# Optimization experiments

Hardware: AMD Instinct MI355X
Metric: run time of the kernel (lower is better)

## Reference

```python
import jax, jax.numpy as jnp
import numpy as np

N = 768          # n_nuclei
EMB = 32         # embedding_dim
RBF = 32         # rbf_dim
CUTOFF = 10.0    # rbf_cutoff
MAXQ = 10        # max(charges)


def _edges(n):
    # fully-connected edge list exactly as in GNN.__call__
    senders = np.arange(n).repeat(n - 1)
    recv = np.arange(n)[None].repeat(n - 1, axis=0)
    recv = (recv + np.arange(n - 1)[:, None] + 1) % n
    return jnp.asarray(senders), jnp.asarray(recv.reshape(-1))


def _mlp2(x, w0, b0, w1, b1=None):
    # AutoMLP(out_dim, depth=2): Dense+silu, Dense (final_bias optional)
    h = jax.nn.silu(x @ w0 + b0)
    y = h @ w1
    return y if b1 is None else y + b1


def _seg_mean(vals, seg, n):
    s = jax.ops.segment_sum(vals, seg, num_segments=n, indices_are_sorted=True)
    c = jax.ops.segment_sum(jnp.ones((vals.shape[0], 1), vals.dtype), seg,
                            num_segments=n, indices_are_sorted=True)
    return s / jnp.maximum(c, 1.0)


def setup_inputs() -> dict:
    key = jax.random.key(0)
    ki = iter(jax.random.split(key, 48))

    def W(din, dout):
        return jax.random.normal(next(ki), (din, dout), jnp.float32) / np.sqrt(din).astype(np.float32)

    def b(d):
        return jax.random.normal(next(ki), (d,), jnp.float32) * 0.01

    return dict(
        nuclei=jax.random.normal(next(ki), (N, 3), jnp.float32) * 3.0,
        charges=jax.random.randint(next(ki), (N,), 0, MAXQ),
        f=(jnp.arange(RBF, dtype=jnp.float32) + 1.0) * jnp.pi,  # BesselRBF param init
        embed_table=jax.random.normal(next(ki), (MAXQ, EMB), jnp.float32),
        mp1_w0=W(96, 32), mp1_b0=b(32), mp1_w1=W(32, 32), mp1_b1=b(32),
        up1_w0=W(64, 64), up1_b0=b(64), up1_w1=W(64, 64), up1_b1=b(64),
        mp2_w0=W(160, 32), mp2_b0=b(32), mp2_w1=W(32, 32), mp2_b1=b(32),
        up2_w0=W(96, 64), up2_b0=b(64), up2_w1=W(64, 64), up2_b1=b(64),
        no_w0=W(160, 3), no_b0=b(3), no_w1=W(3, 3),
        no_embed=jax.random.normal(next(ki), (MAXQ, 3), jnp.float32) * 0.1,
        go_w0=W(160, 1), go_b0=b(1), go_w1=W(1, 1), go_b1=b(1),
    )


def reference(nuclei, charges, f, embed_table,
              mp1_w0, mp1_b0, mp1_w1, mp1_b1,
              up1_w0, up1_b0, up1_w1, up1_b1,
              mp2_w0, mp2_b0, mp2_w1, mp2_b1,
              up2_w0, up2_b0, up2_w1, up2_b1,
              no_w0, no_b0, no_w1, no_embed,
              go_w0, go_b0, go_w1, go_b1):
    nuclei = nuclei.reshape(-1, 3) @ jnp.eye(3, dtype=nuclei.dtype)  # constants 'axes'
    n = nuclei.shape[0]
    senders, receivers = _edges(n)

    # BesselRBF on pairwise distances
    d = jnp.linalg.norm(nuclei[senders] - nuclei[receivers], axis=-1)
    x_ext = d[:, None] + 1e-8
    e_embed = jnp.sqrt(2.0 / CUTOFF) * jnp.sin(f * x_ext / CUTOFF) / x_ext  # [E, RBF]

    n_embed = embed_table[charges]  # [N, EMB]
    embeddings = [n_embed]

    # layer 1: msg out 32, update out 64 (no residual: 32 != 64)
    edge_in = jnp.concatenate([n_embed[senders], n_embed[receivers], e_embed], axis=-1)
    msg = _seg_mean(_mlp2(edge_in, mp1_w0, mp1_b0, mp1_w1, mp1_b1), senders, n)
    upd = _mlp2(jnp.concatenate([n_embed, msg], axis=-1), up1_w0, up1_b0, up1_w1, up1_b1)
    n_embed = upd  # dims differ -> plain replacement
    embeddings.append(n_embed)

    # layer 2: msg out 32, update out 64 (residual: 64 == 64)
    edge_in = jnp.concatenate([n_embed[senders], n_embed[receivers], e_embed], axis=-1)
    msg = _seg_mean(_mlp2(edge_in, mp2_w0, mp2_b0, mp2_w1, mp2_b1), senders, n)
    upd = _mlp2(jnp.concatenate([n_embed, msg], axis=-1), up2_w0, up2_b0, up2_w1, up2_b1)
    n_embed = n_embed + upd
    embeddings.append(n_embed)

    agg = jnp.concatenate(embeddings, axis=-1)  # [N, 32+64+64=160]

    node_out = _mlp2(agg, no_w0, no_b0, no_w1) + no_embed[charges]  # [N, 3]
    global_out = _mlp2(jnp.mean(agg, axis=0), go_w0, go_b0, go_w1, go_b1)  # [1]
    return (node_out, global_out)
```

## Files before the change

kernel.cpp:

```cpp
#include <hip/hip_runtime.h>
#include <hip/hip_bf16.h>

typedef __hip_bfloat16 bf16;
typedef __attribute__((ext_vector_type(8))) short short8;
typedef __attribute__((ext_vector_type(4))) float float4v;

#define NN   768
#define NEPS 767

#define C_NUC   0
#define C_F     2304
#define C_ETAB  2336
#define C_MP1W0 2656
#define C_MP1B0 5728
#define C_MP1W1 5760
#define C_MP1B1 6784
#define C_UP1W0 6816
#define C_UP1B0 10912
#define C_UP1W1 10976
#define C_UP1B1 15072
#define C_MP2W0 15136
#define C_MP2B0 20256
#define C_MP2W1 20288
#define C_MP2B1 21312
#define C_UP2W0 21344
#define C_UP2B0 27488
#define C_UP2W1 27552
#define C_UP2B1 31648
#define C_NOW0  31712
#define C_NOB0  32192
#define C_NOW1  32195
#define C_NOEMB 32204
#define C_GOW0  32234
#define C_GOB0  32394
#define C_GOW1  32395
#define C_GOB1  32396
__device__ float g_c[32400];

#define OFF_EMB0 0
#define OFF_SA1  24576
#define OFF_SB1  49152
#define OFF_MSG1 73728
#define OFF_EMB1 98304
#define OFF_SA2  147456
#define OFF_SB2  172032
#define OFF_MSG2 196608
__device__ float g_ws[221184];
__device__ float g_agg[160];
__device__ int   g_cnt;
__device__ int   g_isf;

struct Ptrs { const void* p[28]; };

__device__ __forceinline__ float b2f(bf16 v){ return __bfloat162float(v); }
__device__ __forceinline__ float LD(const void* p, int i, int f32){
  return f32 ? ((const float*)p)[i] : b2f(((const bf16*)p)[i]);
}
__device__ __forceinline__ int detect_f32(const void* f){
  float v = ((const float*)f)[0];
  return (fabsf(v - 3.14159265f) < 0.01f) ? 1 : 0;
}
__device__ __forceinline__ float fast_rcp(float x){ return __builtin_amdgcn_rcpf(x); }
__device__ __forceinline__ float silu_f(float p){ return p * fast_rcp(1.f + __expf(-p)); }
__device__ __forceinline__ unsigned short rne_bf16(float x){
  unsigned int b = __float_as_uint(x);
  return (unsigned short)((b + 0x7fffu + ((b >> 16) & 1u)) >> 16);
}
__device__ __forceinline__ void cv(const void* p, int off, int sz, int gt, int isf){
  for (int i = gt; i < sz; i += 96*256) g_c[off + i] = LD(p, i, isf);
}

__launch_bounds__(256)
__global__ void k_conv_prep(Ptrs P, const int* __restrict__ charges){
  int t = threadIdx.x;
  int gt = blockIdx.x*256 + t;
  int isf = detect_f32(P.p[2]);
  if (gt == 0){ g_isf = isf; g_cnt = 0; }
  if (gt < 160) g_agg[gt] = 0.f;

  cv(P.p[0],  C_NUC,   2304, gt, isf);
  cv(P.p[2],  C_F,     32,   gt, isf);
  cv(P.p[3],  C_ETAB,  320,  gt, isf);
  cv(P.p[4],  C_MP1W0, 3072, gt, isf);
  cv(P.p[5],  C_MP1B0, 32,   gt, isf);
  cv(P.p[6],  C_MP1W1, 1024, gt, isf);
  cv(P.p[7],  C_MP1B1, 32,   gt, isf);
  cv(P.p[8],  C_UP1W0, 4096, gt, isf);
  cv(P.p[9],  C_UP1B0, 64,   gt, isf);
  cv(P.p[10], C_UP1W1, 4096, gt, isf);
  cv(P.p[11], C_UP1B1, 64,   gt, isf);
  cv(P.p[12], C_MP2W0, 5120, gt, isf);
  cv(P.p[13], C_MP2B0, 32,   gt, isf);
  cv(P.p[14], C_MP2W1, 1024, gt, isf);
  cv(P.p[15], C_MP2B1, 32,   gt, isf);
  cv(P.p[16], C_UP2W0, 6144, gt, isf);
  cv(P.p[17], C_UP2B0, 64,   gt, isf);
  cv(P.p[18], C_UP2W1, 4096, gt, isf);
  cv(P.p[19], C_UP2B1, 64,   gt, isf);
  cv(P.p[20], C_NOW0,  480,  gt, isf);
  cv(P.p[21], C_NOB0,  3,    gt, isf);
  cv(P.p[22], C_NOW1,  9,    gt, isf);
  cv(P.p[23], C_NOEMB, 30,   gt, isf);
  cv(P.p[24], C_GOW0,  160,  gt, isf);
  cv(P.p[25], C_GOB0,  1,    gt, isf);
  cv(P.p[26], C_GOW1,  1,    gt, isf);
  cv(P.p[27], C_GOB1,  1,    gt, isf);

  __shared__ float w0L[2048];
  __shared__ float rowL[8][32];
  for (int idx = t; idx < 2048; idx += 256) w0L[idx] = LD(P.p[4], idx, isf);
  int nd = t >> 5, col = t & 31;
  int node = blockIdx.x*8 + nd;
  int ch = charges[node];
  float v = LD(P.p[3], ch*32 + col, isf);
  g_ws[OFF_EMB0 + node*32 + col] = v;
  rowL[nd][col] = v;
  __syncthreads();
  float sa = 0.f, sb = 0.f;
  #pragma unroll
  for (int k = 0; k < 32; k++){
    float rv = rowL[nd][k];
    sa = fmaf(rv, w0L[k*32 + col],      sa);
    sb = fmaf(rv, w0L[(32+k)*32 + col], sb);
  }
  g_ws[OFF_SA1 + node*32 + col] = sa;
  g_ws[OFF_SB1 + node*32 + col] = sb;
}

__launch_bounds__(256)
__global__ void k_edge(int sa_off, int sb_off, int w0e_off, int b0_off,
                       int w1_off, int b1_off, int msg_off)
{
  __shared__ __align__(16) float pos[NN*3];
  __shared__ __align__(16) float w1L[1024];
  __shared__ float wsum[4][32];
  __shared__ float hsumL[32];

  int i = blockIdx.x, t = threadIdx.x;
  int w = t >> 6, lane = t & 63, q = lane >> 4, c = lane & 15;
  const float* SA = g_ws + sa_off;
  const float* SB = g_ws + sb_off;

  {
    const float4* src = (const float4*)(g_c + C_NUC);
    float4* dst = (float4*)pos;
    for (int idx = t; idx < 576; idx += 256) dst[idx] = src[idx];
    ((float4*)w1L)[t] = ((const float4*)(g_c + w1_off))[t];
  }
  short8 bf0, bf1;
  #pragma unroll
  for (int j = 0; j < 8; j++){
    int row = q*8 + j;
    bf0[j] = (short)rne_bf16(g_c[w0e_off + row*32 + c]);
    bf1[j] = (short)rne_bf16(g_c[w0e_off + row*32 + 16 + c]);
  }
  float preB0 = SA[i*32 + c]      + g_c[b0_off + c];
  float preB1 = SA[i*32 + 16 + c] + g_c[b0_off + 16 + c];
  float fj[8];
  #pragma unroll
  for (int j = 0; j < 8; j++) fj[j] = g_c[C_F + q*8 + j] * 0.1f;
  __syncthreads();

  float px = pos[i*3], py = pos[i*3+1], pz = pos[i*3+2];
  float sum0 = 0.f, sum1 = 0.f;

  for (int tl = w; tl < 48; tl += 4){
    int el = tl*16 + c;
    int ela = (el < NEPS) ? el : 0;
    int r = ela + (ela >= i);
    float dx = px - pos[r*3], dy = py - pos[r*3+1], dz = pz - pos[r*3+2];
    float d  = sqrtf(fmaf(dx, dx, fmaf(dy, dy, dz*dz)));
    float xs = d + 1e-8f;
    float sc = 0.44721359549995793f * fast_rcp(xs);
    short8 af;
    #pragma unroll
    for (int j = 0; j < 8; j++) af[j] = (short)rne_bf16(sc * __sinf(fj[j]*xs));

    float4v z = {0.f, 0.f, 0.f, 0.f};
    float4v a0 = __builtin_amdgcn_mfma_f32_16x16x32_bf16(af, bf0, z, 0, 0, 0);
    float4v a1 = __builtin_amdgcn_mfma_f32_16x16x32_bf16(af, bf1, z, 0, 0, 0);

    #pragma unroll
    for (int p = 0; p < 4; p++){
      int el2 = tl*16 + q*4 + p;
      if (el2 < NEPS){
        int r2 = el2 + (el2 >= i);
        float v0 = a0[p] + preB0 + SB[r2*32 + c];
        float v1 = a1[p] + preB1 + SB[r2*32 + 16 + c];
        sum0 += silu_f(v0);
        sum1 += silu_f(v1);
      }
    }
  }
  sum0 += __shfl_xor(sum0, 16); sum0 += __shfl_xor(sum0, 32);
  sum1 += __shfl_xor(sum1, 16); sum1 += __shfl_xor(sum1, 32);
  if (lane < 16){ wsum[w][lane] = sum0; wsum[w][16 + lane] = sum1; }
  __syncthreads();
  if (t < 32) hsumL[t] = wsum[0][t] + wsum[1][t] + wsum[2][t] + wsum[3][t];
  __syncthreads();
  if (t < 32){
    float y = 0.f;
    #pragma unroll
    for (int m = 0; m < 32; m++) y = fmaf(hsumL[m], w1L[m*32 + t], y);
    g_ws[msg_off + i*32 + t] = y * (1.f/767.f) + g_c[b1_off + t];
  }
}

__launch_bounds__(256)
__global__ void k_upd1(){
  int t = threadIdx.x;
  int nd = t >> 6, col = t & 63;
  int node = blockIdx.x*4 + nd;
  __shared__ __align__(16) float w0L[4096], w1L[4096], m2L[4096];
  __shared__ float catL[4][64], hLL[4][64], e1LL[4][64];
  {
    const float4* s0 = (const float4*)(g_c + C_UP1W0);
    const float4* s1 = (const float4*)(g_c + C_UP1W1);
    const float4* s2 = (const float4*)(g_c + C_MP2W0);
    float4* d0 = (float4*)w0L; float4* d1 = (float4*)w1L; float4* d2 = (float4*)m2L;
    #pragma unroll
    for (int rr = 0; rr < 4; rr++){
      d0[t + rr*256] = s0[t + rr*256];
      d1[t + rr*256] = s1[t + rr*256];
      d2[t + rr*256] = s2[t + rr*256];
    }
  }
  catL[nd][col] = (col < 32) ? g_ws[OFF_EMB0 + node*32 + col]
                             : g_ws[OFF_MSG1 + node*32 + col - 32];
  __syncthreads();
  float a = g_c[C_UP1B0 + col];
  #pragma unroll 8
  for (int k = 0; k < 64; k++) a = fmaf(catL[nd][k], w0L[k*64 + col], a);
  hLL[nd][col] = silu_f(a);
  __syncthreads();
  float y = g_c[C_UP1B1 + col];
  #pragma unroll 8
  for (int k = 0; k < 64; k++) y = fmaf(hLL[nd][k], w1L[k*64 + col], y);
  g_ws[OFF_EMB1 + node*64 + col] = y;
  e1LL[nd][col] = y;
  __syncthreads();
  int c32 = col & 31;
  int base = (col < 32) ? 0 : 2048;
  float s2v = 0.f;
  #pragma unroll 8
  for (int k = 0; k < 64; k++) s2v = fmaf(e1LL[nd][k], m2L[base + k*32 + c32], s2v);
  if (col < 32) g_ws[OFF_SA2 + node*32 + c32] = s2v;
  else          g_ws[OFF_SB2 + node*32 + c32] = s2v;
}

__launch_bounds__(256)
__global__ void k_upd2(const int* __restrict__ charges, void* __restrict__ out){
  int t = threadIdx.x;
  int nd = t >> 6, col = t & 63;
  int node = blockIdx.x*4 + nd;
  __shared__ __align__(16) float w0L[6144], w1L[4096];
  __shared__ float noL[522];
  __shared__ float catL[4][96], hLL[4][64], aggL[4][160], h3L[4][3];
  __shared__ float red[256];
  __shared__ int lastL;
  {
    const float4* s0 = (const float4*)(g_c + C_UP2W0);
    const float4* s1 = (const float4*)(g_c + C_UP2W1);
    float4* d0 = (float4*)w0L; float4* d1 = (float4*)w1L;
    #pragma unroll
    for (int rr = 0; rr < 6; rr++) d0[t + rr*256] = s0[t + rr*256];
    #pragma unroll
    for (int rr = 0; rr < 4; rr++) d1[t + rr*256] = s1[t + rr*256];
    for (int idx = t; idx < 522; idx += 256) noL[idx] = g_c[C_NOW0 + idx];
  }
  catL[nd][col] = g_ws[OFF_EMB1 + node*64 + col];
  if (col < 32){
    catL[nd][64 + col] = g_ws[OFF_MSG2 + node*32 + col];
    aggL[nd][col]      = g_ws[OFF_EMB0 + node*32 + col];
  }
  __syncthreads();
  float a = g_c[C_UP2B0 + col];
  #pragma unroll 8
  for (int k = 0; k < 96; k++) a = fmaf(catL[nd][k], w0L[k*64 + col], a);
  hLL[nd][col] = silu_f(a);
  __syncthreads();
  float y = g_c[C_UP2B1 + col];
  #pragma unroll 8
  for (int k = 0; k < 64; k++) y = fmaf(hLL[nd][k], w1L[k*64 + col], y);
  float e2 = catL[nd][col] + y;
  aggL[nd][32 + col] = catL[nd][col];
  aggL[nd][96 + col] = e2;
  __syncthreads();
  if (col < 3){
    float p = noL[480 + col];
    #pragma unroll 8
    for (int k = 0; k < 160; k++) p = fmaf(aggL[nd][k], noL[k*3 + col], p);
    h3L[nd][col] = silu_f(p);
  }
  __syncthreads();
  if (col < 3){
    float o = 0.f;
    #pragma unroll
    for (int m = 0; m < 3; m++) o = fmaf(h3L[nd][m], noL[483 + m*3 + col], o);
    o += noL[492 + charges[node]*3 + col];
    int isf = g_isf;
    if (isf) ((float*)out)[node*3 + col] = o;
    else     ((bf16*)out)[node*3 + col] = __float2bfloat16(o);
  }
  if (t < 160){
    float s = aggL[0][t] + aggL[1][t] + aggL[2][t] + aggL[3][t];
    atomicAdd(&g_agg[t], s);
  }
  __threadfence();
  __syncthreads();
  if (t == 0){
    int old = atomicAdd(&g_cnt, 1);
    lastL = (old == 191) ? 1 : 0;
  }
  __syncthreads();
  if (lastL){
    float v = 0.f;
    if (t < 160) v = atomicAdd(&g_agg[t], 0.f) * (1.f/768.f) * g_c[C_GOW0 + t];
    red[t] = v;
    __syncthreads();
    if (t == 0){
      float tot = 0.f;
      for (int k = 0; k < 160; k++) tot += red[k];
      float h = silu_f(tot + g_c[C_GOB0]);
      float go = h * g_c[C_GOW1] + g_c[C_GOB1];
      if (g_isf) ((float*)out)[2304] = go;
      else       ((bf16*)out)[2304] = __float2bfloat16(go);
    }
  }
}

extern "C" void kernel_launch(void* const* d_in, const int* in_sizes, int n_in,
                              void* d_out, int out_size, void* d_ws, size_t ws_size,
                              hipStream_t stream) {
  Ptrs P;
  for (int k = 0; k < 28; k++) P.p[k] = d_in[k];
  const int* charges = (const int*)d_in[1];

  k_conv_prep<<<96, 256, 0, stream>>>(P, charges);
  k_edge<<<NN, 256, 0, stream>>>(OFF_SA1, OFF_SB1, C_MP1W0 + 64*32, C_MP1B0,
                                 C_MP1W1, C_MP1B1, OFF_MSG1);
  k_upd1<<<192, 256, 0, stream>>>();
  k_edge<<<NN, 256, 0, stream>>>(OFF_SA2, OFF_SB2, C_MP2W0 + 128*32, C_MP2B0,
                                 C_MP2W1, C_MP2B1, OFF_MSG2);
  k_upd2<<<192, 256, 0, stream>>>(charges, d_out);
}
```

Measured before the change: 189.3 us.

## Fuse node update MLPs into per-node edge kernels, dropping two launches

Each node-update MLP (and the output head plus global reduction) now runs inside the edge kernel block that computed that node's message, so the pipeline goes from five launches to three. The message vector stays in shared memory and the separate update kernels and their workspace buffers are removed. Weights are read straight from global memory, with a split-K reduction across warps. The cost is more redundant weight reads per block (768 blocks instead of 192), and the global-mean atomics now fire once per node rather than once per four nodes.

```diff
diff --git a/kernel.cpp b/kernel.cpp
--- a/kernel.cpp
+++ b/kernel.cpp
@@ -10,7 +10,6 @@
 
 #define C_NUC   0
 #define C_F     2304
-#define C_ETAB  2336
 #define C_MP1W0 2656
 #define C_MP1B0 5728
 #define C_MP1W1 5760
@@ -35,17 +34,15 @@
 #define C_GOB0  32394
 #define C_GOW1  32395
 #define C_GOB1  32396
-__device__ float g_c[32400];
+__device__ __align__(16) float g_c[32400];
 
 #define OFF_EMB0 0
 #define OFF_SA1  24576
 #define OFF_SB1  49152
-#define OFF_MSG1 73728
-#define OFF_EMB1 98304
-#define OFF_SA2  147456
-#define OFF_SB2  172032
-#define OFF_MSG2 196608
-__device__ float g_ws[221184];
+#define OFF_EMB1 73728
+#define OFF_SA2  122880
+#define OFF_SB2  147456
+__device__ float g_ws[172032];
 __device__ float g_agg[160];
 __device__ int   g_cnt;
 __device__ int   g_isf;
@@ -80,7 +77,6 @@
 
   cv(P.p[0],  C_NUC,   2304, gt, isf);
   cv(P.p[2],  C_F,     32,   gt, isf);
-  cv(P.p[3],  C_ETAB,  320,  gt, isf);
   cv(P.p[4],  C_MP1W0, 3072, gt, isf);
   cv(P.p[5],  C_MP1B0, 32,   gt, isf);
   cv(P.p[6],  C_MP1W1, 1024, gt, isf);
@@ -127,200 +123,227 @@
   g_ws[OFF_SB1 + node*32 + col] = sb;
 }
 
+#define EDGE_LOOP(SA_OFF, SB_OFF, W0E, B0, W1, B1)                                   \
+  {                                                                                  \
+    const float* SA = g_ws + (SA_OFF);                                               \
+    const float* SB = g_ws + (SB_OFF);                                               \
+    {                                                                                \
+      const float4* src = (const float4*)(g_c + C_NUC);                              \
+      float4* dst = (float4*)pos;                                                    \
+      for (int idx = t; idx < 576; idx += 256) dst[idx] = src[idx];                  \
+      ((float4*)w1L)[t] = ((const float4*)(g_c + (W1)))[t];                          \
+    }                                                                                \
+    short8 bfr0, bfr1;                                                               \
+    _Pragma("unroll")                                                                \
+    for (int j = 0; j < 8; j++){                                                     \
+      int row = q*8 + j;                                                             \
+      bfr0[j] = (short)rne_bf16(g_c[(W0E) + row*32 + c]);                            \
+      bfr1[j] = (short)rne_bf16(g_c[(W0E) + row*32 + 16 + c]);                       \
+    }                                                                                \
+    float preB0 = SA[i*32 + c]      + g_c[(B0) + c];                                 \
+    float preB1 = SA[i*32 + 16 + c] + g_c[(B0) + 16 + c];                            \
+    float fj[8];                                                                     \
+    _Pragma("unroll")                                                                \
+    for (int j = 0; j < 8; j++) fj[j] = g_c[C_F + q*8 + j] * 0.1f;                   \
+    __syncthreads();                                                                 \
+    float px = pos[i*3], py = pos[i*3+1], pz = pos[i*3+2];                           \
+    float sum0 = 0.f, sum1 = 0.f;                                                    \
+    for (int tl = w; tl < 48; tl += 4){                                              \
+      int el = tl*16 + c;                                                            \
+      int ela = (el < NEPS) ? el : 0;                                                \
+      int r = ela + (ela >= i);                                                      \
+      float dx = px - pos[r*3], dy = py - pos[r*3+1], dz = pz - pos[r*3+2];          \
+      float d  = sqrtf(fmaf(dx, dx, fmaf(dy, dy, dz*dz)));                           \
+      float xs = d + 1e-8f;                                                          \
+      float scv = 0.44721359549995793f * fast_rcp(xs);                               \
+      short8 af;                                                                     \
+      _Pragma("unroll")                                                              \
+      for (int j = 0; j < 8; j++) af[j] = (short)rne_bf16(scv * __sinf(fj[j]*xs));   \
+      float4v z = {0.f, 0.f, 0.f, 0.f};                                              \
+      float4v a0 = __builtin_amdgcn_mfma_f32_16x16x32_bf16(af, bfr0, z, 0, 0, 0);    \
+      float4v a1 = __builtin_amdgcn_mfma_f32_16x16x32_bf16(af, bfr1, z, 0, 0, 0);    \
+      _Pragma("unroll")                                                              \
+      for (int p = 0; p < 4; p++){                                                   \
+        int el2 = tl*16 + q*4 + p;                                                   \
+        if (el2 < NEPS){                                                             \
+          int r2 = el2 + (el2 >= i);                                                 \
+          float v0 = a0[p] + preB0 + SB[r2*32 + c];                                  \
+          float v1 = a1[p] + preB1 + SB[r2*32 + 16 + c];                             \
+          sum0 += silu_f(v0);                                                        \
+          sum1 += silu_f(v1);                                                        \
+        }                                                                            \
+      }                                                                              \
+    }                                                                                \
+    sum0 += __shfl_xor(sum0, 16); sum0 += __shfl_xor(sum0, 32);                      \
+    sum1 += __shfl_xor(sum1, 16); sum1 += __shfl_xor(sum1, 32);                      \
+    if (lane < 16){ wsum[w][lane] = sum0; wsum[w][16 + lane] = sum1; }               \
+    __syncthreads();                                                                 \
+    if (t < 32) hsumL[t] = wsum[0][t] + wsum[1][t] + wsum[2][t] + wsum[3][t];        \
+    __syncthreads();                                                                 \
+    if (t < 32){                                                                     \
+      float y = 0.f;                                                                 \
+      _Pragma("unroll")                                                              \
+      for (int m = 0; m < 32; m++) y = fmaf(hsumL[m], w1L[m*32 + t], y);             \
+      msgL[t] = y * (1.f/767.f) + g_c[(B1) + t];                                     \
+    }                                                                                \
+  }
+
 __launch_bounds__(256)
-__global__ void k_edge(int sa_off, int sb_off, int w0e_off, int b0_off,
-                       int w1_off, int b1_off, int msg_off)
-{
+__global__ void k_edge1(){
   __shared__ __align__(16) float pos[NN*3];
   __shared__ __align__(16) float w1L[1024];
   __shared__ float wsum[4][32];
   __shared__ float hsumL[32];
+  __shared__ float msgL[32];
+  __shared__ float catU[64];
+  __shared__ float hU[64];
+  __shared__ float e1U[64];
+  __shared__ float part[256];
 
   int i = blockIdx.x, t = threadIdx.x;
   int w = t >> 6, lane = t & 63, q = lane >> 4, c = lane & 15;
-  const float* SA = g_ws + sa_off;
-  const float* SB = g_ws + sb_off;
-
-  {
-    const float4* src = (const float4*)(g_c + C_NUC);
-    float4* dst = (float4*)pos;
-    for (int idx = t; idx < 576; idx += 256) dst[idx] = src[idx];
-    ((float4*)w1L)[t] = ((const float4*)(g_c + w1_off))[t];
-  }
-  short8 bf0, bf1;
-  #pragma unroll
-  for (int j = 0; j < 8; j++){
-    int row = q*8 + j;
-    bf0[j] = (short)rne_bf16(g_c[w0e_off + row*32 + c]);
-    bf1[j] = (short)rne_bf16(g_c[w0e_off + row*32 + 16 + c]);
-  }
-  float preB0 = SA[i*32 + c]      + g_c[b0_off + c];
-  float preB1 = SA[i*32 + 16 + c] + g_c[b0_off + 16 + c];
-  float fj[8];
-  #pragma unroll
-  for (int j = 0; j < 8; j++) fj[j] = g_c[C_F + q*8 + j] * 0.1f;
-  __syncthreads();
-
-  float px = pos[i*3], py = pos[i*3+1], pz = pos[i*3+2];
-  float sum0 = 0.f, sum1 = 0.f;
-
-  for (int tl = w; tl < 48; tl += 4){
-    int el = tl*16 + c;
-    int ela = (el < NEPS) ? el : 0;
-    int r = ela + (ela >= i);
-    float dx = px - pos[r*3], dy = py - pos[r*3+1], dz = pz - pos[r*3+2];
-    float d  = sqrtf(fmaf(dx, dx, fmaf(dy, dy, dz*dz)));
-    float xs = d + 1e-8f;
-    float sc = 0.44721359549995793f * fast_rcp(xs);
-    short8 af;
-    #pragma unroll
-    for (int j = 0; j < 8; j++) af[j] = (short)rne_bf16(sc * __sinf(fj[j]*xs));
-
-    float4v z = {0.f, 0.f, 0.f, 0.f};
-    float4v a0 = __builtin_amdgcn_mfma_f32_16x16x32_bf16(af, bf0, z, 0, 0, 0);
-    float4v a1 = __builtin_amdgcn_mfma_f32_16x16x32_bf16(af, bf1, z, 0, 0, 0);
-
-    #pragma unroll
-    for (int p = 0; p < 4; p++){
-      int el2 = tl*16 + q*4 + p;
-      if (el2 < NEPS){
-        int r2 = el2 + (el2 >= i);
-        float v0 = a0[p] + preB0 + SB[r2*32 + c];
-        float v1 = a1[p] + preB1 + SB[r2*32 + 16 + c];
-        sum0 += silu_f(v0);
-        sum1 += silu_f(v1);
-      }
+
+  EDGE_LOOP(OFF_SA1, OFF_SB1, C_MP1W0 + 2048, C_MP1B0, C_MP1W1, C_MP1B1)
+
+  if (t < 32){
+    catU[t] = g_ws[OFF_EMB0 + i*32 + t];
+    catU[32 + t] = msgL[t];
+  }
+  __syncthreads();
+
+  int g = t >> 6, col = t & 63;
+  {
+    const float* w0 = g_c + C_UP1W0;
+    float p0 = 0.f;
+    #pragma unroll
+    for (int j = 0; j < 16; j++){ int k = g*16 + j; p0 = fmaf(catU[k], w0[k*64 + col], p0); }
+    part[t] = p0;
+  }
+  __syncthreads();
+  if (t < 64) hU[t] = silu_f(g_c[C_UP1B0 + t] + part[t] + part[64+t] + part[128+t] + part[192+t]);
+  __syncthreads();
+  {
+    const float* w1u = g_c + C_UP1W1;
+    float p1 = 0.f;
+    #pragma unroll
+    for (int j = 0; j < 16; j++){ int k = g*16 + j; p1 = fmaf(hU[k], w1u[k*64 + col], p1); }
+    part[t] = p1;
+  }
+  __syncthreads();
+  if (t < 64){
+    float y = g_c[C_UP1B1 + t] + part[t] + part[64+t] + part[128+t] + part[192+t];
+    e1U[t] = y;
+    g_ws[OFF_EMB1 + i*64 + t] = y;
+  }
+  __syncthreads();
+  {
+    int half = t >> 7, g2 = (t >> 5) & 3, c32 = t & 31;
+    const float* m2 = g_c + C_MP2W0;
+    float p2 = 0.f;
+    #pragma unroll
+    for (int j = 0; j < 16; j++){
+      int k = g2*16 + j;
+      p2 = fmaf(e1U[k], m2[(half*64 + k)*32 + c32], p2);
     }
-  }
-  sum0 += __shfl_xor(sum0, 16); sum0 += __shfl_xor(sum0, 32);
-  sum1 += __shfl_xor(sum1, 16); sum1 += __shfl_xor(sum1, 32);
-  if (lane < 16){ wsum[w][lane] = sum0; wsum[w][16 + lane] = sum1; }
-  __syncthreads();
-  if (t < 32) hsumL[t] = wsum[0][t] + wsum[1][t] + wsum[2][t] + wsum[3][t];
-  __syncthreads();
-  if (t < 32){
-    float y = 0.f;
-    #pragma unroll
-    for (int m = 0; m < 32; m++) y = fmaf(hsumL[m], w1L[m*32 + t], y);
-    g_ws[msg_off + i*32 + t] = y * (1.f/767.f) + g_c[b1_off + t];
+    part[t] = p2;
+  }
+  __syncthreads();
+  if (t < 64){
+    int half = t >> 5, c32 = t & 31;
+    float s = part[half*128 + c32] + part[half*128 + 32 + c32]
+            + part[half*128 + 64 + c32] + part[half*128 + 96 + c32];
+    if (half == 0) g_ws[OFF_SA2 + i*32 + c32] = s;
+    else           g_ws[OFF_SB2 + i*32 + c32] = s;
   }
 }
 
 __launch_bounds__(256)
-__global__ void k_upd1(){
-  int t = threadIdx.x;
-  int nd = t >> 6, col = t & 63;
-  int node = blockIdx.x*4 + nd;
-  __shared__ __align__(16) float w0L[4096], w1L[4096], m2L[4096];
-  __shared__ float catL[4][64], hLL[4][64], e1LL[4][64];
-  {
-    const float4* s0 = (const float4*)(g_c + C_UP1W0);
-    const float4* s1 = (const float4*)(g_c + C_UP1W1);
-    const float4* s2 = (const float4*)(g_c + C_MP2W0);
-    float4* d0 = (float4*)w0L; float4* d1 = (float4*)w1L; float4* d2 = (float4*)m2L;
-    #pragma unroll
-    for (int rr = 0; rr < 4; rr++){
-      d0[t + rr*256] = s0[t + rr*256];
-      d1[t + rr*256] = s1[t + rr*256];
-      d2[t + rr*256] = s2[t + rr*256];
-    }
-  }
-  catL[nd][col] = (col < 32) ? g_ws[OFF_EMB0 + node*32 + col]
-                             : g_ws[OFF_MSG1 + node*32 + col - 32];
-  __syncthreads();
-  float a = g_c[C_UP1B0 + col];
-  #pragma unroll 8
-  for (int k = 0; k < 64; k++) a = fmaf(catL[nd][k], w0L[k*64 + col], a);
-  hLL[nd][col] = silu_f(a);
-  __syncthreads();
-  float y = g_c[C_UP1B1 + col];
-  #pragma unroll 8
-  for (int k = 0; k < 64; k++) y = fmaf(hLL[nd][k], w1L[k*64 + col], y);
-  g_ws[OFF_EMB1 + node*64 + col] = y;
-  e1LL[nd][col] = y;
-  __syncthreads();
-  int c32 = col & 31;
-  int base = (col < 32) ? 0 : 2048;
-  float s2v = 0.f;
-  #pragma unroll 8
-  for (int k = 0; k < 64; k++) s2v = fmaf(e1LL[nd][k], m2L[base + k*32 + c32], s2v);
-  if (col < 32) g_ws[OFF_SA2 + node*32 + c32] = s2v;
-  else          g_ws[OFF_SB2 + node*32 + c32] = s2v;
-}
-
-__launch_bounds__(256)
-__global__ void k_upd2(const int* __restrict__ charges, void* __restrict__ out){
-  int t = threadIdx.x;
-  int nd = t >> 6, col = t & 63;
-  int node = blockIdx.x*4 + nd;
-  __shared__ __align__(16) float w0L[6144], w1L[4096];
+__global__ void k_edge2(const int* __restrict__ charges, void* __restrict__ out){
+  __shared__ __align__(16) float pos[NN*3];
+  __shared__ __align__(16) float w1L[1024];
+  __shared__ float wsum[4][32];
+  __shared__ float hsumL[32];
+  __shared__ float msgL[32];
+  __shared__ float catU[96];
+  __shared__ float hU[64];
+  __shared__ float aggL[160];
   __shared__ float noL[522];
-  __shared__ float catL[4][96], hLL[4][64], aggL[4][160], h3L[4][3];
-  __shared__ float red[256];
+  __shared__ float h3L[3];
+  __shared__ float part[256];
   __shared__ int lastL;
-  {
-    const float4* s0 = (const float4*)(g_c + C_UP2W0);
-    const float4* s1 = (const float4*)(g_c + C_UP2W1);
-    float4* d0 = (float4*)w0L; float4* d1 = (float4*)w1L;
-    #pragma unroll
-    for (int rr = 0; rr < 6; rr++) d0[t + rr*256] = s0[t + rr*256];
-    #pragma unroll
-    for (int rr = 0; rr < 4; rr++) d1[t + rr*256] = s1[t + rr*256];
-    for (int idx = t; idx < 522; idx += 256) noL[idx] = g_c[C_NOW0 + idx];
-  }
-  catL[nd][col] = g_ws[OFF_EMB1 + node*64 + col];
-  if (col < 32){
-    catL[nd][64 + col] = g_ws[OFF_MSG2 + node*32 + col];
-    aggL[nd][col]      = g_ws[OFF_EMB0 + node*32 + col];
-  }
-  __syncthreads();
-  float a = g_c[C_UP2B0 + col];
-  #pragma unroll 8
-  for (int k = 0; k < 96; k++) a = fmaf(catL[nd][k], w0L[k*64 + col], a);
-  hLL[nd][col] = silu_f(a);
-  __syncthreads();
-  float y = g_c[C_UP2B1 + col];
-  #pragma unroll 8
-  for (int k = 0; k < 64; k++) y = fmaf(hLL[nd][k], w1L[k*64 + col], y);
-  float e2 = catL[nd][col] + y;
-  aggL[nd][32 + col] = catL[nd][col];
-  aggL[nd][96 + col] = e2;
-  __syncthreads();
-  if (col < 3){
-    float p = noL[480 + col];
-    #pragma unroll 8
-    for (int k = 0; k < 160; k++) p = fmaf(aggL[nd][k], noL[k*3 + col], p);
-    h3L[nd][col] = silu_f(p);
-  }
-  __syncthreads();
-  if (col < 3){
+
+  int i = blockIdx.x, t = threadIdx.x;
+  int w = t >> 6, lane = t & 63, q = lane >> 4, c = lane & 15;
+
+  EDGE_LOOP(OFF_SA2, OFF_SB2, C_MP2W0 + 4096, C_MP2B0, C_MP2W1, C_MP2B1)
+
+  if (t < 64) catU[t] = g_ws[OFF_EMB1 + i*64 + t];
+  if (t < 32){ catU[64 + t] = msgL[t]; aggL[t] = g_ws[OFF_EMB0 + i*32 + t]; }
+  for (int idx = t; idx < 522; idx += 256) noL[idx] = g_c[C_NOW0 + idx];
+  __syncthreads();
+
+  int g = t >> 6, col = t & 63;
+  {
+    const float* w0 = g_c + C_UP2W0;
+    float p0 = 0.f;
+    #pragma unroll
+    for (int j = 0; j < 24; j++){ int k = g*24 + j; p0 = fmaf(catU[k], w0[k*64 + col], p0); }
+    part[t] = p0;
+  }
+  __syncthreads();
+  if (t < 64) hU[t] = silu_f(g_c[C_UP2B0 + t] + part[t] + part[64+t] + part[128+t] + part[192+t]);
+  __syncthreads();
+  {
+    const float* w1u = g_c + C_UP2W1;
+    float p1 = 0.f;
+    #pragma unroll
+    for (int j = 0; j < 16; j++){ int k = g*16 + j; p1 = fmaf(hU[k], w1u[k*64 + col], p1); }
+    part[t] = p1;
+  }
+  __syncthreads();
+  if (t < 64){
+    float y = g_c[C_UP2B1 + t] + part[t] + part[64+t] + part[128+t] + part[192+t];
+    float e2 = catU[t] + y;
+    aggL[32 + t] = catU[t];
+    aggL[96 + t] = e2;
+  }
+  __syncthreads();
+  if (t < 48){
+    int chunk = t / 3, c3 = t - chunk*3;
+    float p = 0.f;
+    #pragma unroll
+    for (int j = 0; j < 10; j++){ int k = chunk*10 + j; p = fmaf(aggL[k], noL[k*3 + c3], p); }
+    part[t] = p;
+  }
+  __syncthreads();
+  if (t < 3){
+    float p = noL[480 + t];
+    #pragma unroll
+    for (int ch = 0; ch < 16; ch++) p += part[ch*3 + t];
+    h3L[t] = silu_f(p);
+  }
+  __syncthreads();
+  if (t < 3){
     float o = 0.f;
     #pragma unroll
-    for (int m = 0; m < 3; m++) o = fmaf(h3L[nd][m], noL[483 + m*3 + col], o);
-    o += noL[492 + charges[node]*3 + col];
-    int isf = g_isf;
-    if (isf) ((float*)out)[node*3 + col] = o;
-    else     ((bf16*)out)[node*3 + col] = __float2bfloat16(o);
-  }
-  if (t < 160){
-    float s = aggL[0][t] + aggL[1][t] + aggL[2][t] + aggL[3][t];
-    atomicAdd(&g_agg[t], s);
-  }
+    for (int m = 0; m < 3; m++) o = fmaf(h3L[m], noL[483 + m*3 + t], o);
+    o += noL[492 + charges[i]*3 + t];
+    if (g_isf) ((float*)out)[i*3 + t] = o;
+    else       ((bf16*)out)[i*3 + t] = __float2bfloat16(o);
+  }
+  if (t < 160) atomicAdd(&g_agg[t], aggL[t]);
   __threadfence();
   __syncthreads();
-  if (t == 0){
-    int old = atomicAdd(&g_cnt, 1);
-    lastL = (old == 191) ? 1 : 0;
-  }
+  if (t == 0) lastL = (atomicAdd(&g_cnt, 1) == NN - 1) ? 1 : 0;
   __syncthreads();
   if (lastL){
     float v = 0.f;
     if (t < 160) v = atomicAdd(&g_agg[t], 0.f) * (1.f/768.f) * g_c[C_GOW0 + t];
-    red[t] = v;
+    part[t] = v;
     __syncthreads();
     if (t == 0){
       float tot = 0.f;
-      for (int k = 0; k < 160; k++) tot += red[k];
+      for (int k = 0; k < 160; k++) tot += part[k];
       float h = silu_f(tot + g_c[C_GOB0]);
       float go = h * g_c[C_GOW1] + g_c[C_GOB1];
       if (g_isf) ((float*)out)[2304] = go;
@@ -337,10 +360,6 @@
   const int* charges = (const int*)d_in[1];
 
   k_conv_prep<<<96, 256, 0, stream>>>(P, charges);
-  k_edge<<<NN, 256, 0, stream>>>(OFF_SA1, OFF_SB1, C_MP1W0 + 64*32, C_MP1B0,
-                                 C_MP1W1, C_MP1B1, OFF_MSG1);
-  k_upd1<<<192, 256, 0, stream>>>();
-  k_edge<<<NN, 256, 0, stream>>>(OFF_SA2, OFF_SB2, C_MP2W0 + 128*32, C_MP2B0,
-                                 C_MP2W1, C_MP2B1, OFF_MSG2);
-  k_upd2<<<192, 256, 0, stream>>>(charges, d_out);
-}
+  k_edge1<<<NN, 256, 0, stream>>>();
+  k_edge2<<<NN, 256, 0, stream>>>(charges, d_out);
+}
```

After: 221.2 us. 16.8% more time.
